# Performance work log

Measured on AMD Instinct MI355X. Metric: run time of the kernel, lower is better.

Reference implementation:

```python
import jax, jax.numpy as jnp
import numpy as np

EMBED = 1024
HEADS = 16
HEAD_DIM = 64
FF = 4096
EPS = 1e-5


def _layernorm(x, g, b):
    mu = jnp.mean(x, axis=-1, keepdims=True)
    var = jnp.mean(jnp.square(x - mu), axis=-1, keepdims=True)
    return (x - mu) * jax.lax.rsqrt(var + EPS) * g + b


def setup_inputs() -> dict:
    key = jax.random.key(0)
    ks = jax.random.split(key, 12)
    s_in = 1.0 / np.sqrt(EMBED)
    s_hd = 1.0 / np.sqrt(HEADS * HEAD_DIM)
    s_ff = 1.0 / np.sqrt(FF)
    return {
        "x": jax.random.normal(ks[0], (4, 2048, EMBED), dtype=jnp.float32),
        "Wq": jax.random.uniform(ks[1], (HEADS, EMBED, HEAD_DIM), jnp.float32, -s_in, s_in),
        "Wk": jax.random.uniform(ks[2], (HEADS, EMBED, HEAD_DIM), jnp.float32, -s_in, s_in),
        "Wv": jax.random.uniform(ks[3], (HEADS, EMBED, HEAD_DIM), jnp.float32, -s_in, s_in),
        "Wo": jax.random.uniform(ks[4], (HEADS * HEAD_DIM, EMBED), jnp.float32, -s_hd, s_hd),
        "bo": jax.random.uniform(ks[5], (EMBED,), jnp.float32, -s_hd, s_hd),
        "W1": jax.random.uniform(ks[6], (EMBED, FF), jnp.float32, -s_in, s_in),
        "b1": jax.random.uniform(ks[7], (FF,), jnp.float32, -s_in, s_in),
        "W2": jax.random.uniform(ks[8], (FF, EMBED), jnp.float32, -s_ff, s_ff),
        "b2": jax.random.uniform(ks[9], (EMBED,), jnp.float32, -s_ff, s_ff),
        "ln1_g": jnp.ones((EMBED,), jnp.float32),
        "ln1_b": jnp.zeros((EMBED,), jnp.float32),
        "ln2_g": jnp.ones((EMBED,), jnp.float32),
        "ln2_b": jnp.zeros((EMBED,), jnp.float32),
    }


def reference(x, Wq, Wk, Wv, Wo, bo, W1, b1, W2, b2, ln1_g, ln1_b, ln2_g, ln2_b):
    B, T, C = x.shape
    h = _layernorm(x, ln1_g, ln1_b)
    # per-head projections, batched over heads: [B,H,T,Dh]
    q = jnp.einsum("btc,hcd->bhtd", h, Wq)
    k = jnp.einsum("btc,hcd->bhtd", h, Wk)
    v = jnp.einsum("btc,hcd->bhtd", h, Wv)
    scale = HEAD_DIM ** -0.5
    att = jnp.einsum("bhtd,bhsd->bhts", q, k) * scale  # [B,H,T,T]
    causal = jnp.tril(jnp.ones((T, T), dtype=bool))
    att = jnp.where(causal, att, -jnp.inf)
    att = jax.nn.softmax(att, axis=-1)
    out = jnp.einsum("bhts,bhsd->bhtd", att, v)  # [B,H,T,Dh]
    # concat heads (matches torch.cat over head outputs) -> [B,T,H*Dh]
    out = out.transpose(0, 2, 1, 3).reshape(B, T, HEADS * HEAD_DIM)
    x = x + out @ Wo + bo
    h2 = _layernorm(x, ln2_g, ln2_b)
    ff = jax.nn.relu(h2 @ W1 + b1) @ W2 + b2
    return x + ff
```

## Files before the change

kernel.cpp:

```cpp
#include <hip/hip_runtime.h>
#include <hip/hip_bf16.h>

#define EMBED 1024
#define HEADS 16
#define HEAD_DIM 64
#define FFDIM 4096
#define TSEQ 2048
#define BATCH 4
#define ROWS (BATCH * TSEQ)

typedef __bf16 bf16;
typedef __attribute__((ext_vector_type(8))) __bf16 bf16x8;
typedef __attribute__((ext_vector_type(4))) __bf16 bf16x4;
typedef __attribute__((ext_vector_type(4))) float f32x4;

typedef const __attribute__((address_space(1))) void* gvp;
typedef __attribute__((address_space(3))) void* svp;

__global__ __launch_bounds__(256) void conv_wqkv_t(
    const float* __restrict__ Wq, const float* __restrict__ Wk,
    const float* __restrict__ Wv, bf16* __restrict__ WqkvT) {
  __shared__ bf16 t[64][72];
  int tid = threadIdx.x;
  int k0 = blockIdx.x * 64;
  int head = blockIdx.y;
  int which = blockIdx.z;
  const float* src = which == 0 ? Wq : which == 1 ? Wk : Wv;
  float scale = which == 0 ? 0.125f * 1.44269504088896f : 1.0f;
  src += (size_t)head * 65536;
  bf16* dst = WqkvT + ((size_t)which * 1024 + head * 64) * 1024;
#pragma unroll
  for (int i = 0; i < 4; ++i) {
    int r = i * 16 + (tid >> 4);
    int c = (tid & 15) * 4;
    float4 v = *(const float4*)&src[(size_t)(k0 + r) * 64 + c];
    t[c + 0][r] = (bf16)(v.x * scale);
    t[c + 1][r] = (bf16)(v.y * scale);
    t[c + 2][r] = (bf16)(v.z * scale);
    t[c + 3][r] = (bf16)(v.w * scale);
  }
  __syncthreads();
#pragma unroll
  for (int i = 0; i < 2; ++i) {
    int r = i * 32 + (tid >> 3);
    int c = (tid & 7) * 8;
    bf16x8 o;
#pragma unroll
    for (int j = 0; j < 8; ++j) o[j] = t[r][c + j];
    *(bf16x8*)&dst[(size_t)r * 1024 + k0 + c] = o;
  }
}

__global__ __launch_bounds__(256) void transpose_conv(
    const float* __restrict__ W, bf16* __restrict__ WT, int K, int N) {
  __shared__ bf16 t[64][72];
  int tid = threadIdx.x;
  int n0 = blockIdx.x * 64, k0 = blockIdx.y * 64;
#pragma unroll
  for (int i = 0; i < 4; ++i) {
    int r = i * 16 + (tid >> 4);
    int c = (tid & 15) * 4;
    float4 v = *(const float4*)&W[(size_t)(k0 + r) * N + n0 + c];
    t[c + 0][r] = (bf16)v.x;
    t[c + 1][r] = (bf16)v.y;
    t[c + 2][r] = (bf16)v.z;
    t[c + 3][r] = (bf16)v.w;
  }
  __syncthreads();
#pragma unroll
  for (int i = 0; i < 2; ++i) {
    int r = i * 32 + (tid >> 3);
    int c = (tid & 7) * 8;
    bf16x8 o;
#pragma unroll
    for (int j = 0; j < 8; ++j) o[j] = t[r][c + j];
    *(bf16x8*)&WT[(size_t)(n0 + r) * K + k0 + c] = o;
  }
}

__global__ __launch_bounds__(256) void transpose_v(const bf16* __restrict__ v,
                                                   bf16* __restrict__ vt) {
  __shared__ bf16 t[64][72];
  int bh = blockIdx.y;
  int t0 = blockIdx.x * 64;
  const bf16* src = v + (size_t)bh * 131072;
  bf16* dst = vt + (size_t)bh * 131072;
  int tid = threadIdx.x;
#pragma unroll
  for (int i = 0; i < 2; ++i) {
    int c = tid + i * 256;
    int r = c >> 3, d0 = (c & 7) * 8;
    bf16x8 vv = *(const bf16x8*)&src[(size_t)(t0 + r) * 64 + d0];
#pragma unroll
    for (int j = 0; j < 8; ++j) t[d0 + j][r] = vv[j];
  }
  __syncthreads();
#pragma unroll
  for (int i = 0; i < 2; ++i) {
    int c = tid + i * 256;
    int r = c >> 3, s0 = (c & 7) * 8;
    bf16x8 o;
#pragma unroll
    for (int j = 0; j < 8; ++j) o[j] = t[r][s0 + j];
    *(bf16x8*)&dst[(size_t)r * 2048 + t0 + s0] = o;
  }
}

__global__ __launch_bounds__(256) void ln_kernel(
    const float* __restrict__ x, const float* __restrict__ g,
    const float* __restrict__ bta, bf16* __restrict__ out) {
  int row = blockIdx.x;
  const float* xr = x + (size_t)row * EMBED;
  float4 v = ((const float4*)xr)[threadIdx.x];
  float s1 = v.x + v.y + v.z + v.w;
  float s2 = v.x * v.x + v.y * v.y + v.z * v.z + v.w * v.w;
#pragma unroll
  for (int off = 1; off < 64; off <<= 1) {
    s1 += __shfl_xor(s1, off);
    s2 += __shfl_xor(s2, off);
  }
  __shared__ float red[8];
  int wid = threadIdx.x >> 6;
  int lane = threadIdx.x & 63;
  if (lane == 0) {
    red[wid * 2] = s1;
    red[wid * 2 + 1] = s2;
  }
  __syncthreads();
  s1 = red[0] + red[2] + red[4] + red[6];
  s2 = red[1] + red[3] + red[5] + red[7];
  float mu = s1 * (1.0f / EMBED);
  float var = s2 * (1.0f / EMBED) - mu * mu;
  float rs = rsqrtf(var + 1e-5f);
  float4 gv = ((const float4*)g)[threadIdx.x];
  float4 bv = ((const float4*)bta)[threadIdx.x];
  bf16x4 o;
  o[0] = (bf16)((v.x - mu) * rs * gv.x + bv.x);
  o[1] = (bf16)((v.y - mu) * rs * gv.y + bv.y);
  o[2] = (bf16)((v.z - mu) * rs * gv.z + bv.z);
  o[3] = (bf16)((v.w - mu) * rs * gv.w + bv.w);
  *(bf16x4*)(out + (size_t)row * EMBED + threadIdx.x * 4) = o;
}

template <int EPI>
__global__ __launch_bounds__(512, 2) void gemm256(
    const bf16* __restrict__ A, const bf16* __restrict__ BT,
    bf16* __restrict__ Cb, const float* __restrict__ bias, int M, int N,
    int K) {
  __shared__ __attribute__((aligned(16))) char lds[98304];
  int gx = gridDim.x;
  int nwg = gx * gridDim.y;
  int wgid = blockIdx.y * gx + blockIdx.x;
  int cpx = nwg >> 3;
  int swz = (wgid & 7) * cpx + (wgid >> 3);
  int m0 = (swz / gx) * 256, n0 = (swz % gx) * 256;
  int tid = threadIdx.x;
  int lane = tid & 63, wid = tid >> 6;
  int lr = lane & 15, lg = lane >> 4;
  int wrM = (wid >> 2) * 128;
  int wcN = (wid & 3) * 64;
  int crow = lane >> 2;
  int slotg = (lane & 3) ^ (crow & 3);
  int NT = K >> 5;
  size_t rb = (size_t)K * 2;

  auto stageT = [&](int t) {
    char* dst = lds + ((unsigned)t % 3u) * 32768u;
#pragma unroll
    for (int q = 0; q < 2; ++q) {
      int c = wid * 2 + q;
      const char* srcA = (const char*)A + (size_t)(m0 + c * 16 + crow) * rb +
                         (size_t)t * 64 + slotg * 16;
      __builtin_amdgcn_global_load_lds((gvp)srcA, (svp)(dst + c * 1024), 16, 0,
                                       0);
      const char* srcB = (const char*)BT + (size_t)(n0 + c * 16 + crow) * rb +
                         (size_t)t * 64 + slotg * 16;
      __builtin_amdgcn_global_load_lds((gvp)srcB, (svp)(dst + 16384 + c * 1024),
                                       16, 0, 0);
    }
  };

  stageT(0);
  stageT(1);
  f32x4 acc[8][4] = {};
  int swcol = ((lg ^ (lr & 3)) * 16);
  for (int t = 0; t < NT; ++t) {
    asm volatile("s_waitcnt vmcnt(4)" ::: "memory");
    __builtin_amdgcn_s_barrier();
    const char* Ab = lds + ((unsigned)t % 3u) * 32768u;
    const char* Bb = Ab + 16384;
    bf16x8 af[8], bfr[4];
#pragma unroll
    for (int j = 0; j < 4; ++j)
      bfr[j] = *(const bf16x8*)(Bb + (wcN + j * 16 + lr) * 64 + swcol);
#pragma unroll
    for (int i = 0; i < 8; ++i)
      af[i] = *(const bf16x8*)(Ab + (wrM + i * 16 + lr) * 64 + swcol);
    int tn = t + 2;
    stageT(tn < NT ? tn : tn - NT);
    __builtin_amdgcn_s_setprio(1);
#pragma unroll
    for (int i = 0; i < 8; ++i)
#pragma unroll
      for (int j = 0; j < 4; ++j)
        acc[i][j] = __builtin_amdgcn_mfma_f32_16x16x32_bf16(af[i], bfr[j],
                                                            acc[i][j], 0, 0, 0);
    __builtin_amdgcn_s_setprio(0);
  }
  asm volatile("s_waitcnt vmcnt(0)" ::: "memory");
#pragma unroll
  for (int i = 0; i < 8; ++i) {
#pragma unroll
    for (int j = 0; j < 4; ++j) {
#pragma unroll
      for (int r = 0; r < 4; ++r) {
        int row = m0 + wrM + i * 16 + lg * 4 + r;
        int col = n0 + wcN + j * 16 + lr;
        float v = acc[i][j][r];
        if (EPI == 0) {
          int which = col >> 10, cc = col & 1023;
          int b = row >> 11, tt = row & 2047, h = cc >> 6, d = cc & 63;
          bf16* dst = Cb + (size_t)which * 8388608;
          dst[((size_t)((b << 4) + h) * TSEQ + tt) * HEAD_DIM + d] = (bf16)v;
        } else {
          size_t o = (size_t)row * N + col;
          float u = v + bias[col];
          Cb[o] = (bf16)(u > 0.f ? u : 0.f);
        }
      }
    }
  }
}

template <int EPI>
__global__ __launch_bounds__(256) void gemm_bf16(
    const bf16* __restrict__ A, const bf16* __restrict__ BT,
    float* __restrict__ Cf, bf16* __restrict__ Cb,
    const float* __restrict__ bias, const float* __restrict__ resid, int M,
    int N, int K) {
  __shared__ __attribute__((aligned(16))) bf16 As[128 * 32];
  __shared__ __attribute__((aligned(16))) bf16 Bs[128 * 32];
  int gx = gridDim.x;
  int nwg = gx * gridDim.y;
  int wgid = blockIdx.y * gx + blockIdx.x;
  int cpx = nwg >> 3;
  int swz = (wgid & 7) * cpx + (wgid >> 3);
  int m0 = (swz / gx) * 128, n0 = (swz % gx) * 128;
  int tid = threadIdx.x;
  int lane = tid & 63, wid = tid >> 6;
  int lr = lane & 15, lg = lane >> 4;
  int wr = (wid >> 1) * 64, wc = (wid & 1) * 64;
  int srow = lane >> 2;
  int sk = (lane & 3) * 8;
  f32x4 acc[4][4] = {};
  for (int kt = 0; kt < K; kt += 32) {
#pragma unroll
    for (int i = 0; i < 2; ++i) {
      int c = wid * 2 + i;
      int row = c * 16 + srow;
      const bf16* ga = &A[(size_t)(m0 + row) * K + kt + sk];
      const bf16* gb = &BT[(size_t)(n0 + row) * K + kt + sk];
      __builtin_amdgcn_global_load_lds((gvp)(const void*)ga,
                                       (svp)(void*)&As[c * 512], 16, 0, 0);
      __builtin_amdgcn_global_load_lds((gvp)(const void*)gb,
                                       (svp)(void*)&Bs[c * 512], 16, 0, 0);
    }
    __syncthreads();
    bf16x8 af[4], bfr[4];
#pragma unroll
    for (int i = 0; i < 4; ++i) {
      af[i] = *(const bf16x8*)&As[(wr + i * 16 + lr) * 32 + lg * 8];
      bfr[i] = *(const bf16x8*)&Bs[(wc + i * 16 + lr) * 32 + lg * 8];
    }
#pragma unroll
    for (int ar = 0; ar < 4; ++ar)
#pragma unroll
      for (int br = 0; br < 4; ++br)
        acc[ar][br] = __builtin_amdgcn_mfma_f32_16x16x32_bf16(
            af[ar], bfr[br], acc[ar][br], 0, 0, 0);
    __syncthreads();
  }
#pragma unroll
  for (int ar = 0; ar < 4; ++ar) {
#pragma unroll
    for (int br = 0; br < 4; ++br) {
#pragma unroll
      for (int r = 0; r < 4; ++r) {
        int row = m0 + wr + ar * 16 + lg * 4 + r;
        int col = n0 + wc + br * 16 + lr;
        float v = acc[ar][br][r];
        size_t o = (size_t)row * N + col;
        Cf[o] = resid[o] + bias[col] + v;
      }
    }
  }
}

__global__ __launch_bounds__(256) void attn_kernel(
    const bf16* __restrict__ q, const bf16* __restrict__ k,
    const bf16* __restrict__ vt, bf16* __restrict__ out) {
  __shared__ __attribute__((aligned(16))) bf16 Ks[64][68];
  __shared__ __attribute__((aligned(16))) bf16 Vs[64][68];
  __shared__ __attribute__((aligned(16))) bf16 Ps[4][32][68];
  int bh = blockIdx.x;
  int b = bh >> 4, h = bh & 15;
  const bf16* qb = q + (size_t)bh * TSEQ * HEAD_DIM;
  const bf16* kb = k + (size_t)bh * TSEQ * HEAD_DIM;
  const bf16* vb = vt + (size_t)bh * HEAD_DIM * TSEQ;
  int tid = threadIdx.x, lane = tid & 63, w = tid >> 6;
  int lr = lane & 15, lg = lane >> 4;
  int Q = 15 - blockIdx.y;
  int tw = Q * 128 + w * 32;
  bf16x8 aq[2][2];
#pragma unroll
  for (int rg = 0; rg < 2; ++rg)
#pragma unroll
    for (int kc = 0; kc < 2; ++kc)
      aq[rg][kc] = *(const bf16x8*)&qb[(size_t)(tw + rg * 16 + lr) * HEAD_DIM +
                                       kc * 32 + lg * 8];
  f32x4 o[2][4] = {};
  float lrow[2][4] = {};
  int nj = 2 * Q + 2;
  for (int j = 0; j < nj; ++j) {
#pragma unroll
    for (int i = 0; i < 2; ++i) {
      int c = tid + i * 256;
      int rr = c >> 3, ko = (c & 7) * 8;
      *(bf16x8*)&Ks[rr][ko] =
          *(const bf16x8*)&kb[(size_t)(j * 64 + rr) * HEAD_DIM + ko];
      *(bf16x8*)&Vs[rr][ko] =
          *(const bf16x8*)&vb[(size_t)rr * TSEQ + j * 64 + ko];
    }
    __syncthreads();
    f32x4 s[2][4] = {};
#pragma unroll
    for (int nb = 0; nb < 4; ++nb) {
#pragma unroll
      for (int kc = 0; kc < 2; ++kc) {
        bf16x8 bk = *(const bf16x8*)&Ks[nb * 16 + lr][kc * 32 + lg * 8];
        s[0][nb] = __builtin_amdgcn_mfma_f32_16x16x32_bf16(aq[0][kc], bk,
                                                           s[0][nb], 0, 0, 0);
        s[1][nb] = __builtin_amdgcn_mfma_f32_16x16x32_bf16(aq[1][kc], bk,
                                                           s[1][nb], 0, 0, 0);
      }
    }
    if (j >= 2 * Q) {
#pragma unroll
      for (int rg = 0; rg < 2; ++rg)
#pragma unroll
        for (int nb = 0; nb < 4; ++nb)
#pragma unroll
          for (int r = 0; r < 4; ++r) {
            int sg = j * 64 + nb * 16 + lr;
            int tg = tw + rg * 16 + lg * 4 + r;
            if (sg > tg) s[rg][nb][r] = -1e30f;
          }
    }
#pragma unroll
    for (int rg = 0; rg < 2; ++rg) {
      float p[4][4];
#pragma unroll
      for (int r = 0; r < 4; ++r) {
        float su = 0.f;
#pragma unroll
        for (int nb = 0; nb < 4; ++nb) {
          p[nb][r] = exp2f(s[rg][nb][r] - 8.0f);
          su += p[nb][r];
        }
#pragma unroll
        for (int off = 1; off < 16; off <<= 1) su += __shfl_xor(su, off);
        lrow[rg][r] += su;
      }
#pragma unroll
      for (int nb = 0; nb < 4; ++nb)
#pragma unroll
        for (int r = 0; r < 4; ++r)
          Ps[w][rg * 16 + lg * 4 + r][nb * 16 + lr] = (bf16)p[nb][r];
    }
#pragma unroll
    for (int kc = 0; kc < 2; ++kc) {
      bf16x8 pa0 = *(const bf16x8*)&Ps[w][lr][kc * 32 + lg * 8];
      bf16x8 pa1 = *(const bf16x8*)&Ps[w][16 + lr][kc * 32 + lg * 8];
#pragma unroll
      for (int br = 0; br < 4; ++br) {
        bf16x8 bv = *(const bf16x8*)&Vs[br * 16 + lr][kc * 32 + lg * 8];
        o[0][br] =
            __builtin_amdgcn_mfma_f32_16x16x32_bf16(pa0, bv, o[0][br], 0, 0, 0);
        o[1][br] =
            __builtin_amdgcn_mfma_f32_16x16x32_bf16(pa1, bv, o[1][br], 0, 0, 0);
      }
    }
    __syncthreads();
  }
#pragma unroll
  for (int rg = 0; rg < 2; ++rg)
#pragma unroll
    for (int br = 0; br < 4; ++br)
#pragma unroll
      for (int r = 0; r < 4; ++r) {
        int t = tw + rg * 16 + lg * 4 + r;
        int d = br * 16 + lr;
        float val = o[rg][br][r] / lrow[rg][r];
        out[((size_t)(b * TSEQ) + t) * EMBED + h * HEAD_DIM + d] = (bf16)val;
      }
}

extern "C" void kernel_launch(void* const* d_in, const int* in_sizes, int n_in,
                              void* d_out, int out_size, void* d_ws,
                              size_t ws_size, hipStream_t stream) {
  const float* x = (const float*)d_in[0];
  const float* Wq = (const float*)d_in[1];
  const float* Wk = (const float*)d_in[2];
  const float* Wv = (const float*)d_in[3];
  const float* Wo = (const float*)d_in[4];
  const float* bo = (const float*)d_in[5];
  const float* W1 = (const float*)d_in[6];
  const float* b1 = (const float*)d_in[7];
  const float* W2 = (const float*)d_in[8];
  const float* b2 = (const float*)d_in[9];
  const float* g1 = (const float*)d_in[10];
  const float* be1 = (const float*)d_in[11];
  const float* g2 = (const float*)d_in[12];
  const float* be2 = (const float*)d_in[13];
  float* out = (float*)d_out;
  char* ws = (char*)d_ws;

  const size_t U = 16777216;
  bf16* h = (bf16*)(ws + 0 * U);
  bf16* qb = (bf16*)(ws + 1 * U);
  bf16* vtb = (bf16*)(ws + 0 * U);
  bf16* vnb = (bf16*)(ws + 3 * U);
  bf16* ao = (bf16*)(ws + 3 * U);
  float* x1 = (float*)(ws + 4 * U);
  bf16* h2 = (bf16*)(ws + 6 * U);
  bf16* ff1 = (bf16*)(ws + 0 * U);
  char* wbase = ws + 7 * U;
  bf16* WqkvT = (bf16*)(wbase);
  bf16* WoT = (bf16*)(wbase + 6291456);
  bf16* W1T = (bf16*)(wbase + 8388608);
  bf16* W2T = (bf16*)(wbase + 16777216);

  hipLaunchKernelGGL(conv_wqkv_t, dim3(16, 16, 3), dim3(256), 0, stream, Wq,
                     Wk, Wv, WqkvT);
  hipLaunchKernelGGL(transpose_conv, dim3(16, 16), dim3(256), 0, stream, Wo,
                     WoT, 1024, 1024);
  hipLaunchKernelGGL(transpose_conv, dim3(64, 16), dim3(256), 0, stream, W1,
                     W1T, 1024, 4096);
  hipLaunchKernelGGL(transpose_conv, dim3(16, 64), dim3(256), 0, stream, W2,
                     W2T, 4096, 1024);
  hipLaunchKernelGGL(ln_kernel, dim3(8192), dim3(256), 0, stream, x, g1, be1,
                     h);
  hipLaunchKernelGGL((gemm256<0>), dim3(12, 32), dim3(512), 0, stream, h,
                     WqkvT, qb, (const float*)nullptr, ROWS, 3072, 1024);
  hipLaunchKernelGGL(transpose_v, dim3(32, 64), dim3(256), 0, stream, vnb,
                     vtb);
  hipLaunchKernelGGL(attn_kernel, dim3(64, 16), dim3(256), 0, stream, qb,
                     qb + 8388608, vtb, ao);
  hipLaunchKernelGGL((gemm_bf16<2>), dim3(8, 64), dim3(256), 0, stream, ao,
                     WoT, x1, (bf16*)nullptr, bo, x, ROWS, 1024, 1024);
  hipLaunchKernelGGL(ln_kernel, dim3(8192), dim3(256), 0, stream, x1, g2, be2,
                     h2);
  hipLaunchKernelGGL((gemm256<3>), dim3(16, 32), dim3(512), 0, stream, h2, W1T,
                     ff1, b1, ROWS, 4096, 1024);
  hipLaunchKernelGGL((gemm_bf16<2>), dim3(8, 64), dim3(256), 0, stream, ff1,
                     W2T, out, (bf16*)nullptr, b2, x1, ROWS, 1024, 4096);
}
```

Baseline: 466.2 us.

## Split GEMM main loop into two half-tile phases with interleaved A/B staging

The GEMM K-loop is restructured into two phases per tile. Each phase loads half of the A fragments, issues either the A or the B async global->LDS stage for tile t+2, then runs 16 MFMAs, with extra barriers and sched_barriers pinning the order. Occupancy hint drops from 2 to 1 workgroup per CU so more registers are available. The redundant wraparound prefetch on the last iterations is removed, and the final wait is vmcnt(0). The changes aim to interleave memory issue with MFMA work and keep register pressure lower, at the cost of extra barriers and possibly less latency hiding from a second resident workgroup.

```diff
diff --git a/kernel.cpp b/kernel.cpp
--- a/kernel.cpp
+++ b/kernel.cpp
@@ -143,7 +143,7 @@
 }
 
 template <int EPI>
-__global__ __launch_bounds__(512, 2) void gemm256(
+__global__ __launch_bounds__(512, 1) void gemm256(
     const bf16* __restrict__ A, const bf16* __restrict__ BT,
     bf16* __restrict__ Cb, const float* __restrict__ bias, int M, int N,
     int K) {
@@ -164,7 +164,7 @@
   int NT = K >> 5;
   size_t rb = (size_t)K * 2;
 
-  auto stageT = [&](int t) {
+  auto stageA = [&](int t) {
     char* dst = lds + ((unsigned)t % 3u) * 32768u;
 #pragma unroll
     for (int q = 0; q < 2; ++q) {
@@ -173,41 +173,72 @@
                          (size_t)t * 64 + slotg * 16;
       __builtin_amdgcn_global_load_lds((gvp)srcA, (svp)(dst + c * 1024), 16, 0,
                                        0);
+    }
+  };
+  auto stageB = [&](int t) {
+    char* dst = lds + ((unsigned)t % 3u) * 32768u + 16384u;
+#pragma unroll
+    for (int q = 0; q < 2; ++q) {
+      int c = wid * 2 + q;
       const char* srcB = (const char*)BT + (size_t)(n0 + c * 16 + crow) * rb +
                          (size_t)t * 64 + slotg * 16;
-      __builtin_amdgcn_global_load_lds((gvp)srcB, (svp)(dst + 16384 + c * 1024),
-                                       16, 0, 0);
+      __builtin_amdgcn_global_load_lds((gvp)srcB, (svp)(dst + c * 1024), 16, 0,
+                                       0);
     }
   };
 
-  stageT(0);
-  stageT(1);
+  stageA(0);
+  stageB(0);
+  stageA(1);
+  stageB(1);
   f32x4 acc[8][4] = {};
   int swcol = ((lg ^ (lr & 3)) * 16);
   for (int t = 0; t < NT; ++t) {
-    asm volatile("s_waitcnt vmcnt(4)" ::: "memory");
+    if (t == NT - 1)
+      asm volatile("s_waitcnt vmcnt(0)" ::: "memory");
+    else
+      asm volatile("s_waitcnt vmcnt(4)" ::: "memory");
     __builtin_amdgcn_s_barrier();
+    __builtin_amdgcn_sched_barrier(0);
     const char* Ab = lds + ((unsigned)t % 3u) * 32768u;
     const char* Bb = Ab + 16384;
-    bf16x8 af[8], bfr[4];
+    int tn = t + 2;
+    bool st = tn < NT;
+    bf16x8 bfr[4], afA[4], afB[4];
 #pragma unroll
     for (int j = 0; j < 4; ++j)
       bfr[j] = *(const bf16x8*)(Bb + (wcN + j * 16 + lr) * 64 + swcol);
 #pragma unroll
-    for (int i = 0; i < 8; ++i)
-      af[i] = *(const bf16x8*)(Ab + (wrM + i * 16 + lr) * 64 + swcol);
-    int tn = t + 2;
-    stageT(tn < NT ? tn : tn - NT);
+    for (int i = 0; i < 4; ++i)
+      afA[i] = *(const bf16x8*)(Ab + (wrM + i * 16 + lr) * 64 + swcol);
+    if (st) stageA(tn);
+    __builtin_amdgcn_s_barrier();
+    __builtin_amdgcn_sched_barrier(0);
     __builtin_amdgcn_s_setprio(1);
 #pragma unroll
-    for (int i = 0; i < 8; ++i)
+    for (int i = 0; i < 4; ++i)
 #pragma unroll
       for (int j = 0; j < 4; ++j)
-        acc[i][j] = __builtin_amdgcn_mfma_f32_16x16x32_bf16(af[i], bfr[j],
+        acc[i][j] = __builtin_amdgcn_mfma_f32_16x16x32_bf16(afA[i], bfr[j],
                                                             acc[i][j], 0, 0, 0);
     __builtin_amdgcn_s_setprio(0);
-  }
-  asm volatile("s_waitcnt vmcnt(0)" ::: "memory");
+    __builtin_amdgcn_sched_barrier(0);
+#pragma unroll
+    for (int i = 0; i < 4; ++i)
+      afB[i] = *(const bf16x8*)(Ab + (wrM + 64 + i * 16 + lr) * 64 + swcol);
+    if (st) stageB(tn);
+    __builtin_amdgcn_s_barrier();
+    __builtin_amdgcn_sched_barrier(0);
+    __builtin_amdgcn_s_setprio(1);
+#pragma unroll
+    for (int i = 0; i < 4; ++i)
+#pragma unroll
+      for (int j = 0; j < 4; ++j)
+        acc[4 + i][j] = __builtin_amdgcn_mfma_f32_16x16x32_bf16(
+            afB[i], bfr[j], acc[4 + i][j], 0, 0, 0);
+    __builtin_amdgcn_s_setprio(0);
+    __builtin_amdgcn_sched_barrier(0);
+  }
 #pragma unroll
   for (int i = 0; i < 8; ++i) {
 #pragma unroll
```

New measurement: 458.6 us. About the same (-1.6%).
